# Kernel tuning notes

Hardware: AMD Instinct MI355X
Metric: run time of the kernel (lower is better)

The kernel has to match this reference:

```python
import jax, jax.numpy as jnp
import numpy as np

EXPERTS, IN_DIM, OUT_DIM, BATCH = 8, 1024, 1024, 16384

def setup_inputs() -> dict:
    key = jax.random.key(0)
    k1, k2, k3, k4 = jax.random.split(key, 4)
    bound = np.sqrt(6.0 / (IN_DIM * OUT_DIM)).astype(np.float32)
    bbound = np.sqrt(6.0 / (1 * OUT_DIM)).astype(np.float32)
    return {
        "x": jax.random.normal(k1, (BATCH, IN_DIM), dtype=jnp.float32),
        "weights": jax.random.uniform(k2, (BATCH, EXPERTS), dtype=jnp.float32),
        "W": jax.random.uniform(k3, (EXPERTS, IN_DIM, OUT_DIM), jnp.float32, -bound, bound),
        "b": jax.random.uniform(k4, (EXPERTS, 1, OUT_DIM), jnp.float32, -bbound, bbound),
    }

def reference(x, weights, W, b):
    # y[b,o] = sum_e weights[b,e] * (x[b,:] @ W[e] + b[e])
    # Fused triple einsum avoids materializing the [B,E,O] intermediate.
    y = jnp.einsum("be,bi,eio->bo", weights, x, W)
    y = y + jnp.einsum("be,eo->bo", weights, b[:, 0, :])
    return y
```

## Files before the change

### kernel.cpp

```cpp
#include <hip/hip_runtime.h>
#include <hip/hip_bf16.h>
#include <stdint.h>

#define BATCH   16384
#define EXPERTS 8
#define IN_DIM  1024
#define OUT_DIM 1024

typedef unsigned short u16;
typedef short  bf16x8 __attribute__((ext_vector_type(8)));
typedef float  f32x4  __attribute__((ext_vector_type(4)));

__device__ __forceinline__ u16 f2bf(float f) {
  uint32_t u = __float_as_uint(f);
  u += 0x7fffu + ((u >> 16) & 1u);
  return (u16)(u >> 16);
}

#define GLDS16(g, l)                                                      \
  __builtin_amdgcn_global_load_lds(                                       \
      (const __attribute__((address_space(1))) void*)(g),                 \
      (__attribute__((address_space(3))) void*)(l), 16, 0, 0)

#define MFMA_BF16 __builtin_amdgcn_mfma_f32_16x16x32_bf16
#define SB0 __builtin_amdgcn_sched_barrier(0)
#define LGKM(N) asm volatile("s_waitcnt lgkmcnt(" #N ")" ::: "memory")

__global__ void cvt_x(const float* __restrict__ x, u16* __restrict__ xb) {
  size_t i = ((size_t)blockIdx.x * 256 + threadIdx.x) * 4;
  float4 v = *reinterpret_cast<const float4*>(x + i);
  ushort4 o;
  o.x = f2bf(v.x); o.y = f2bf(v.y); o.z = f2bf(v.z); o.w = f2bf(v.w);
  *reinterpret_cast<ushort4*>(xb + i) = o;
}

__global__ void cvt_w(const float* __restrict__ W, u16* __restrict__ wbt) {
  __shared__ u16 t[64][72];
  const int e  = blockIdx.z;
  const int i0 = blockIdx.x * 64;
  const int o0 = blockIdx.y * 64;
  const int tid = threadIdx.x;
  const int c  = (tid & 15) * 4;
  const int r_ = tid >> 4;
  const float* src = W + ((size_t)e << 20);
#pragma unroll
  for (int p = 0; p < 4; ++p) {
    int r = r_ + p * 16;
    float4 v = *reinterpret_cast<const float4*>(src + (size_t)(i0 + r) * 1024 + o0 + c);
    t[r][c + 0] = f2bf(v.x); t[r][c + 1] = f2bf(v.y);
    t[r][c + 2] = f2bf(v.z); t[r][c + 3] = f2bf(v.w);
  }
  __syncthreads();
  u16* dst = wbt + ((size_t)e << 20);
#pragma unroll
  for (int p = 0; p < 4; ++p) {
    int orow = r_ + p * 16;
    ushort4 u;
    u.x = t[c + 0][orow]; u.y = t[c + 1][orow];
    u.z = t[c + 2][orow]; u.w = t[c + 3][orow];
    *reinterpret_cast<ushort4*>(dst + (size_t)(o0 + orow) * 1024 + i0 + c) = u;
  }
}

__global__ __launch_bounds__(512, 2)
void zgemm(const u16* __restrict__ xb, const u16* __restrict__ wbt,
           const float* __restrict__ wts, const float* __restrict__ bias,
           float* __restrict__ y) {
  __shared__ u16 sm[69632];
  char* smb = (char*)sm;
  float* rl = (float*)(sm + 65536);

  const int tid = threadIdx.x;
  const int l   = tid & 63;
  const int w   = tid >> 6;
  const int wm  = w >> 2;
  const int wn  = w & 3;
  const int x8  = blockIdx.x & 7;
  const int jj  = blockIdx.x >> 3;
  const int n0  = (x8 >> 1) * 256;
  const int b0  = (((x8 & 1) << 5) + jj) << 8;

#pragma unroll
  for (int i = 0; i < 4; ++i) {
    const int flat = tid + i * 512;
    const int e = flat & 7, r = flat >> 3;
    const float* wr = wts + (size_t)(b0 + r) * EXPERTS;
    float we = fmaxf(wr[e], 1e-20f);
    float rr = (e < 7) ? we / fmaxf(wr[e + 1], 1e-20f) : we;
    rl[e * 256 + r] = rr;
  }

  const int rb    = (w << 3) + (l >> 3);
  const int chunk = ((l & 7) ^ (l >> 3)) << 3;
  const u16* pAg = xb  + (size_t)(b0 + rb) * IN_DIM + chunk;
  const u16* pBg = wbt + (size_t)(n0 + rb) * 1024 + chunk;

  const int l15  = l & 15;
  const int kb0  = (((l >> 4) << 4)) ^ ((l & 7) << 4);
  const int arow = (wm * 128 + l15) * 128;
  const int brow = (wn * 64 + l15) * 128;
  const int wlo  = (wm << 9) + ((l >> 4) << 4);

  f32x4 acc[8][4];
#pragma unroll
  for (int m = 0; m < 8; ++m)
#pragma unroll
    for (int n = 0; n < 4; ++n) acc[m][n] = (f32x4){0.f, 0.f, 0.f, 0.f};

#define STG_A(q, dstE, ev_kv)                                              \
  GLDS16(pAg + (size_t)((q) * 64) * 1024 + (ev_kv),                        \
         sm + (dstE) + (q) * 4096 + (w << 9))
#define STG_B(q, dstE, off)                                                \
  GLDS16(pBg + (off) + (size_t)((q) * 64) * 1024,                          \
         sm + (dstE) + (q) * 4096 + (w << 9))

  STG_A(0, 0, 0); STG_A(1, 0, 0); STG_A(2, 0, 0); STG_A(3, 0, 0);
  STG_B(0, 32768, 0); STG_B(1, 32768, 0); STG_B(2, 32768, 0); STG_B(3, 32768, 0);
  asm volatile("s_waitcnt vmcnt(0)" ::: "memory");
  LGKM(0);
  __builtin_amdgcn_s_barrier();

#define MM(AV, BV, MB)                                                     \
  __builtin_amdgcn_s_setprio(1);                                           \
  _Pragma("unroll")                                                        \
  for (int m = 0; m < 4; ++m)                                              \
    _Pragma("unroll")                                                      \
    for (int n = 0; n < 4; ++n)                                            \
      acc[(MB) + m][n] = MFMA_BF16(AV[m], BV[n], acc[(MB) + m][n], 0, 0, 0); \
  __builtin_amdgcn_s_setprio(0);

#pragma unroll 1
  for (int t = 0; t < 128; ++t) {
    const int tn  = (t + 1) & 127;
    const int e1  = tn >> 4, k1 = tn & 15;
    const int ArB = (t & 1) << 15;
    const int AwE = ((t + 1) & 1) << 14;
    const int BrB = 65536 + ((t & 1) << 15);
    const int BwE = 32768 + (((t + 1) & 1) << 14);
    const size_t aoffg = (size_t)k1 * 64;
    const size_t boffg = (size_t)e1 * 1048576 + (size_t)k1 * 64;

    bf16x8 a0[4], b0v[4], a1[4], a2v[4], b1v[4], a3[4];

#pragma unroll
    for (int m = 0; m < 4; ++m)
      a0[m] = *(const bf16x8*)(smb + ArB + arow + m * 2048 + kb0);
#pragma unroll
    for (int n = 0; n < 4; ++n)
      b0v[n] = *(const bf16x8*)(smb + BrB + brow + n * 2048 + kb0);
#pragma unroll
    for (int m = 0; m < 4; ++m)
      a1[m] = *(const bf16x8*)(smb + ArB + arow + (m + 4) * 2048 + kb0);
    STG_A(0, AwE, aoffg); STG_A(1, AwE, aoffg);
    STG_A(2, AwE, aoffg); STG_A(3, AwE, aoffg);
    STG_B(0, BwE, boffg); STG_B(1, BwE, boffg);
    STG_B(2, BwE, boffg); STG_B(3, BwE, boffg);

    LGKM(4); SB0;
#pragma unroll
    for (int m = 0; m < 4; ++m)
      a2v[m] = *(const bf16x8*)(smb + ArB + arow + m * 2048 + (kb0 ^ 64));
#pragma unroll
    for (int n = 0; n < 4; ++n)
      b1v[n] = *(const bf16x8*)(smb + BrB + brow + n * 2048 + (kb0 ^ 64));
    MM(a0, b0v, 0)

    LGKM(8); SB0;
#pragma unroll
    for (int m = 0; m < 4; ++m)
      a3[m] = *(const bf16x8*)(smb + ArB + arow + (m + 4) * 2048 + (kb0 ^ 64));
    MM(a1, b0v, 4)

    LGKM(4); SB0;
    MM(a2v, b1v, 0)

    LGKM(0); SB0;
    MM(a3, b1v, 4)

    asm volatile("s_waitcnt vmcnt(0)" ::: "memory");
    __builtin_amdgcn_s_barrier();

    if ((t & 15) == 15 && t != 127) {
      const int e = t >> 4;
#pragma unroll
      for (int m = 0; m < 8; ++m) {
        const f32x4 rv = *(const f32x4*)(smb + 131072 + e * 1024 + wlo + m * 64);
#pragma unroll
        for (int n = 0; n < 4; ++n) acc[m][n] *= rv;
      }
      LGKM(0); SB0;
    }
  }
  asm volatile("s_waitcnt vmcnt(0)" ::: "memory");

  float bv[4][8];
#pragma unroll
  for (int n = 0; n < 4; ++n) {
    const int c = n0 + wn * 64 + n * 16 + l15;
#pragma unroll
    for (int ee = 0; ee < 8; ++ee) bv[n][ee] = bias[ee * OUT_DIM + c];
  }
#pragma unroll
  for (int m = 0; m < 8; ++m) {
    const f32x4 rv7 = *(const f32x4*)(smb + 131072 + 7 * 1024 + wlo + m * 64);
    const int r0 = b0 + wm * 128 + m * 16 + ((l >> 4) << 2);
#pragma unroll
    for (int j = 0; j < 4; ++j) {
      const float* wr = wts + (size_t)(r0 + j) * EXPERTS;
      float w8[8];
#pragma unroll
      for (int ee = 0; ee < 8; ++ee) w8[ee] = wr[ee];
#pragma unroll
      for (int n = 0; n < 4; ++n) {
        const int c = n0 + wn * 64 + n * 16 + l15;
        float v = acc[m][n][j] * rv7[j];
#pragma unroll
        for (int ee = 0; ee < 8; ++ee) v += w8[ee] * bv[n][ee];
        y[(size_t)(r0 + j) * OUT_DIM + c] = v;
      }
    }
  }
}

extern "C" void kernel_launch(void* const* d_in, const int* in_sizes, int n_in,
                              void* d_out, int out_size, void* d_ws, size_t ws_size,
                              hipStream_t stream) {
  const float* x    = (const float*)d_in[0];
  const float* wts  = (const float*)d_in[1];
  const float* W    = (const float*)d_in[2];
  const float* bias = (const float*)d_in[3];
  float* y = (float*)d_out;

  const size_t xb_elems = (size_t)BATCH * IN_DIM;
  const size_t wb_elems = (size_t)EXPERTS * IN_DIM * OUT_DIM;
  if (ws_size < (xb_elems + wb_elems) * sizeof(u16)) return;
  u16* xb  = (u16*)d_ws;
  u16* wbt = xb + xb_elems;

  cvt_x<<<(BATCH * IN_DIM) / (4 * 256), 256, 0, stream>>>(x, xb);
  cvt_w<<<dim3(IN_DIM / 64, OUT_DIM / 64, EXPERTS), 256, 0, stream>>>(W, wbt);
  zgemm<<<dim3(256), 512, 0, stream>>>(xb, wbt, wts, bias, y);
}
```

Measured before the change: 259.7 us.

## Prefetch next tile's first fragments across the barrier in GEMM main loop

Moves the vmcnt wait and barrier to mid-iteration so the first A/B LDS fragments of the next K-step can be read before the last two MFMA groups of the current step. This hides LDS read latency at the start of each iteration. An extra barrier is added at the end of each iteration to protect buffer reuse. The expert rescale block now loads all ratio vectors before multiplying. The added barrier and changed lgkm counts risk extra stalls or ordering hazards.

```diff
diff --git a/kernel.cpp b/kernel.cpp
--- a/kernel.cpp
+++ b/kernel.cpp
@@ -25,6 +25,7 @@
 #define MFMA_BF16 __builtin_amdgcn_mfma_f32_16x16x32_bf16
 #define SB0 __builtin_amdgcn_sched_barrier(0)
 #define LGKM(N) asm volatile("s_waitcnt lgkmcnt(" #N ")" ::: "memory")
+#define VM0     asm volatile("s_waitcnt vmcnt(0)" ::: "memory")
 
 __global__ void cvt_x(const float* __restrict__ x, u16* __restrict__ xb) {
   size_t i = ((size_t)blockIdx.x * 256 + threadIdx.x) * 4;
@@ -114,12 +115,6 @@
   GLDS16(pBg + (off) + (size_t)((q) * 64) * 1024,                          \
          sm + (dstE) + (q) * 4096 + (w << 9))
 
-  STG_A(0, 0, 0); STG_A(1, 0, 0); STG_A(2, 0, 0); STG_A(3, 0, 0);
-  STG_B(0, 32768, 0); STG_B(1, 32768, 0); STG_B(2, 32768, 0); STG_B(3, 32768, 0);
-  asm volatile("s_waitcnt vmcnt(0)" ::: "memory");
-  LGKM(0);
-  __builtin_amdgcn_s_barrier();
-
 #define MM(AV, BV, MB)                                                     \
   __builtin_amdgcn_s_setprio(1);                                           \
   _Pragma("unroll")                                                        \
@@ -129,32 +124,42 @@
       acc[(MB) + m][n] = MFMA_BF16(AV[m], BV[n], acc[(MB) + m][n], 0, 0, 0); \
   __builtin_amdgcn_s_setprio(0);
 
+  STG_A(0, 0, 0); STG_A(1, 0, 0); STG_A(2, 0, 0); STG_A(3, 0, 0);
+  STG_B(0, 32768, 0); STG_B(1, 32768, 0); STG_B(2, 32768, 0); STG_B(3, 32768, 0);
+  VM0;
+  LGKM(0);
+  __builtin_amdgcn_s_barrier();
+
+  bf16x8 a0[4], b0v[4];
+#pragma unroll
+  for (int m = 0; m < 4; ++m)
+    a0[m] = *(const bf16x8*)(smb + arow + m * 2048 + kb0);
+#pragma unroll
+  for (int n = 0; n < 4; ++n)
+    b0v[n] = *(const bf16x8*)(smb + 65536 + brow + n * 2048 + kb0);
+
 #pragma unroll 1
   for (int t = 0; t < 128; ++t) {
     const int tn  = (t + 1) & 127;
     const int e1  = tn >> 4, k1 = tn & 15;
-    const int ArB = (t & 1) << 15;
-    const int AwE = ((t + 1) & 1) << 14;
-    const int BrB = 65536 + ((t & 1) << 15);
-    const int BwE = 32768 + (((t + 1) & 1) << 14);
+    const int ArB  = (t & 1) << 15;
+    const int BrB  = 65536 + ((t & 1) << 15);
+    const int ArBn = ((t + 1) & 1) << 15;
+    const int BrBn = 65536 + (((t + 1) & 1) << 15);
+    const int AwE  = ((t + 1) & 1) << 14;
+    const int BwE  = 32768 + (((t + 1) & 1) << 14);
     const size_t aoffg = (size_t)k1 * 64;
     const size_t boffg = (size_t)e1 * 1048576 + (size_t)k1 * 64;
 
-    bf16x8 a0[4], b0v[4], a1[4], a2v[4], b1v[4], a3[4];
-
-#pragma unroll
-    for (int m = 0; m < 4; ++m)
-      a0[m] = *(const bf16x8*)(smb + ArB + arow + m * 2048 + kb0);
-#pragma unroll
-    for (int n = 0; n < 4; ++n)
-      b0v[n] = *(const bf16x8*)(smb + BrB + brow + n * 2048 + kb0);
-#pragma unroll
-    for (int m = 0; m < 4; ++m)
-      a1[m] = *(const bf16x8*)(smb + ArB + arow + (m + 4) * 2048 + kb0);
+    bf16x8 a1[4], a2v[4], b1v[4], a3[4];
+
     STG_A(0, AwE, aoffg); STG_A(1, AwE, aoffg);
     STG_A(2, AwE, aoffg); STG_A(3, AwE, aoffg);
     STG_B(0, BwE, boffg); STG_B(1, BwE, boffg);
     STG_B(2, BwE, boffg); STG_B(3, BwE, boffg);
+#pragma unroll
+    for (int m = 0; m < 4; ++m)
+      a1[m] = *(const bf16x8*)(smb + ArB + arow + (m + 4) * 2048 + kb0);
 
     LGKM(4); SB0;
 #pragma unroll
@@ -171,27 +176,36 @@
       a3[m] = *(const bf16x8*)(smb + ArB + arow + (m + 4) * 2048 + (kb0 ^ 64));
     MM(a1, b0v, 4)
 
+    VM0;
+    __builtin_amdgcn_s_barrier();
+
     LGKM(4); SB0;
+#pragma unroll
+    for (int m = 0; m < 4; ++m)
+      a0[m] = *(const bf16x8*)(smb + ArBn + arow + m * 2048 + kb0);
+#pragma unroll
+    for (int n = 0; n < 4; ++n)
+      b0v[n] = *(const bf16x8*)(smb + BrBn + brow + n * 2048 + kb0);
     MM(a2v, b1v, 0)
 
-    LGKM(0); SB0;
+    LGKM(8); SB0;
     MM(a3, b1v, 4)
-
-    asm volatile("s_waitcnt vmcnt(0)" ::: "memory");
-    __builtin_amdgcn_s_barrier();
 
     if ((t & 15) == 15 && t != 127) {
       const int e = t >> 4;
-#pragma unroll
-      for (int m = 0; m < 8; ++m) {
-        const f32x4 rv = *(const f32x4*)(smb + 131072 + e * 1024 + wlo + m * 64);
-#pragma unroll
-        for (int n = 0; n < 4; ++n) acc[m][n] *= rv;
-      }
+      f32x4 rv[8];
+#pragma unroll
+      for (int m = 0; m < 8; ++m)
+        rv[m] = *(const f32x4*)(smb + 131072 + e * 1024 + wlo + m * 64);
       LGKM(0); SB0;
+#pragma unroll
+      for (int m = 0; m < 8; ++m)
+#pragma unroll
+        for (int n = 0; n < 4; ++n) acc[m][n] *= rv[m];
     }
-  }
-  asm volatile("s_waitcnt vmcnt(0)" ::: "memory");
+    __builtin_amdgcn_s_barrier();
+  }
+  VM0; LGKM(0);
 
   float bv[4][8];
 #pragma unroll
```

Result: slower. 283.4 us (+9.1%).

## Prepack W into MFMA fragment layout and load B directly to registers

Applied to the files above, without the earlier changes.

The weight conversion kernel now writes W in a layout that matches the MFMA operand fragments, so the GEMM loads B straight from global memory into registers and no longer stages it through LDS. LDS use drops to the A tiles only, and the main loop is unrolled by two with register double-buffering of B and reworked waits and barriers. Launch bounds change to one block per SM. Each wave fetches its own B fragments, with no sharing through LDS, so global or L2 traffic for B rises, and occupancy hints change.

```diff
diff --git a/kernel.cpp b/kernel.cpp
--- a/kernel.cpp
+++ b/kernel.cpp
@@ -25,6 +25,7 @@
 #define MFMA_BF16 __builtin_amdgcn_mfma_f32_16x16x32_bf16
 #define SB0 __builtin_amdgcn_sched_barrier(0)
 #define LGKM(N) asm volatile("s_waitcnt lgkmcnt(" #N ")" ::: "memory")
+#define VMC(N)  asm volatile("s_waitcnt vmcnt(" #N ")" ::: "memory")
 
 __global__ void cvt_x(const float* __restrict__ x, u16* __restrict__ xb) {
   size_t i = ((size_t)blockIdx.x * 256 + threadIdx.x) * 4;
@@ -34,41 +35,46 @@
   *reinterpret_cast<ushort4*>(xb + i) = o;
 }
 
-__global__ void cvt_w(const float* __restrict__ W, u16* __restrict__ wbt) {
-  __shared__ u16 t[64][72];
-  const int e  = blockIdx.z;
-  const int i0 = blockIdx.x * 64;
-  const int o0 = blockIdx.y * 64;
-  const int tid = threadIdx.x;
-  const int c  = (tid & 15) * 4;
-  const int r_ = tid >> 4;
-  const float* src = W + ((size_t)e << 20);
-#pragma unroll
-  for (int p = 0; p < 4; ++p) {
-    int r = r_ + p * 16;
-    float4 v = *reinterpret_cast<const float4*>(src + (size_t)(i0 + r) * 1024 + o0 + c);
-    t[r][c + 0] = f2bf(v.x); t[r][c + 1] = f2bf(v.y);
-    t[r][c + 2] = f2bf(v.z); t[r][c + 3] = f2bf(v.w);
+__global__ void cvt_wp(const float* __restrict__ W, u16* __restrict__ wtp) {
+  __shared__ u16 tl[64][260];
+  const int kt = blockIdx.x, og = blockIdx.y, e = blockIdx.z;
+  const int t = threadIdx.x;
+  const float* src = W + ((size_t)e << 20) + (size_t)kt * 64 * 1024 + og * 256;
+#pragma unroll
+  for (int p = 0; p < 16; ++p) {
+    int flat = p * 256 + t;
+    int i  = flat >> 6;
+    int o4 = (flat & 63) * 4;
+    float4 v = *reinterpret_cast<const float4*>(src + (size_t)i * 1024 + o4);
+    tl[i][o4 + 0] = f2bf(v.x); tl[i][o4 + 1] = f2bf(v.y);
+    tl[i][o4 + 2] = f2bf(v.z); tl[i][o4 + 3] = f2bf(v.w);
   }
   __syncthreads();
-  u16* dst = wbt + ((size_t)e << 20);
-#pragma unroll
-  for (int p = 0; p < 4; ++p) {
-    int orow = r_ + p * 16;
-    ushort4 u;
-    u.x = t[c + 0][orow]; u.y = t[c + 1][orow];
-    u.z = t[c + 2][orow]; u.w = t[c + 3][orow];
-    *reinterpret_cast<ushort4*>(dst + (size_t)(o0 + orow) * 1024 + i0 + c) = u;
-  }
-}
-
-__global__ __launch_bounds__(512, 2)
-void zgemm(const u16* __restrict__ xb, const u16* __restrict__ wbt,
+  u16* dst = wtp + (size_t)(e * 16 + kt) * 65536 + (size_t)og * 16 * 1024;
+#pragma unroll
+  for (int s = 0; s < 8; ++s) {
+    int c   = s * 256 + t;
+    int obl = c >> 7;
+    int kf  = (c >> 6) & 1;
+    int ln  = c & 63;
+    int ol  = obl * 16 + (ln & 15);
+    int ib  = kf * 32 + ((ln >> 4) << 3);
+    u16 buf[8];
+#pragma unroll
+    for (int j = 0; j < 8; ++j) buf[j] = tl[ib + j][ol];
+    u16* d = dst + (size_t)obl * 1024 + kf * 512 + ln * 8;
+    *reinterpret_cast<ushort4*>(d)     = *(ushort4*)&buf[0];
+    *reinterpret_cast<ushort4*>(d + 4) = *(ushort4*)&buf[4];
+  }
+}
+
+__global__ __launch_bounds__(512, 1)
+void zgemm(const u16* __restrict__ xb, const u16* __restrict__ wtp,
            const float* __restrict__ wts, const float* __restrict__ bias,
            float* __restrict__ y) {
-  __shared__ u16 sm[69632];
-  char* smb = (char*)sm;
-  float* rl = (float*)(sm + 65536);
+  __shared__ u16 sm[36864];
+  const char* smb = (const char*)sm;
+  float* rl = (float*)(sm + 32768);
 
   const int tid = threadIdx.x;
   const int l   = tid & 63;
@@ -90,35 +96,27 @@
     rl[e * 256 + r] = rr;
   }
 
-  const int rb    = (w << 3) + (l >> 3);
+  const int rbl   = (w << 3) + (l >> 3);
   const int chunk = ((l & 7) ^ (l >> 3)) << 3;
-  const u16* pAg = xb  + (size_t)(b0 + rb) * IN_DIM + chunk;
-  const u16* pBg = wbt + (size_t)(n0 + rb) * 1024 + chunk;
+  const u16* pAg = xb + (size_t)(b0 + rbl) * IN_DIM + chunk;
 
   const int l15  = l & 15;
   const int kb0  = (((l >> 4) << 4)) ^ ((l & 7) << 4);
   const int arow = (wm * 128 + l15) * 128;
-  const int brow = (wn * 64 + l15) * 128;
   const int wlo  = (wm << 9) + ((l >> 4) << 4);
 
+  const int obBase = (n0 >> 4) + wn * 4;
+  const u16* pBf = wtp + (size_t)obBase * 1024 + (size_t)l * 8;
+
   f32x4 acc[8][4];
 #pragma unroll
   for (int m = 0; m < 8; ++m)
 #pragma unroll
     for (int n = 0; n < 4; ++n) acc[m][n] = (f32x4){0.f, 0.f, 0.f, 0.f};
 
-#define STG_A(q, dstE, ev_kv)                                              \
-  GLDS16(pAg + (size_t)((q) * 64) * 1024 + (ev_kv),                        \
+#define STG_A(q, dstE, kv)                                                 \
+  GLDS16(pAg + (size_t)((q) * 64) * 1024 + (size_t)(kv) * 64,              \
          sm + (dstE) + (q) * 4096 + (w << 9))
-#define STG_B(q, dstE, off)                                                \
-  GLDS16(pBg + (off) + (size_t)((q) * 64) * 1024,                          \
-         sm + (dstE) + (q) * 4096 + (w << 9))
-
-  STG_A(0, 0, 0); STG_A(1, 0, 0); STG_A(2, 0, 0); STG_A(3, 0, 0);
-  STG_B(0, 32768, 0); STG_B(1, 32768, 0); STG_B(2, 32768, 0); STG_B(3, 32768, 0);
-  asm volatile("s_waitcnt vmcnt(0)" ::: "memory");
-  LGKM(0);
-  __builtin_amdgcn_s_barrier();
 
 #define MM(AV, BV, MB)                                                     \
   __builtin_amdgcn_s_setprio(1);                                           \
@@ -129,69 +127,82 @@
       acc[(MB) + m][n] = MFMA_BF16(AV[m], BV[n], acc[(MB) + m][n], 0, 0, 0); \
   __builtin_amdgcn_s_setprio(0);
 
+  bf16x8 a0[4];
+  bf16x8 bEk0[4], bEk1[4], bOk0[4], bOk1[4];
+
+  STG_A(0, 0, 0); STG_A(1, 0, 0); STG_A(2, 0, 0); STG_A(3, 0, 0);
+#pragma unroll
+  for (int nf = 0; nf < 4; ++nf) {
+    bEk0[nf] = *(const bf16x8*)(pBf + (size_t)nf * 1024);
+    bEk1[nf] = *(const bf16x8*)(pBf + (size_t)nf * 1024 + 512);
+  }
+  VMC(0);
+  LGKM(0);
+  __builtin_amdgcn_s_barrier();
+#pragma unroll
+  for (int m = 0; m < 4; ++m)
+    a0[m] = *(const bf16x8*)(smb + arow + m * 2048 + kb0);
+
+#define BODY(TT, BCk0, BCk1, BNk0, BNk1, ARB, AWE)                         \
+  {                                                                        \
+    const int tn = ((TT) + 1) & 127;                                       \
+    const int e1 = tn >> 4, k1 = tn & 15;                                  \
+    bf16x8 a1[4], a2[4], a3[4];                                            \
+                 \
+    STG_A(0, AWE, k1); STG_A(1, AWE, k1); STG_A(2, AWE, k1); STG_A(3, AWE, k1); \
+    SB0;                                                                   \
+    {                                                                      \
+      const u16* pb = pBf + (size_t)(e1 * 16 + k1) * 65536;                \
+      _Pragma("unroll")                                                    \
+      for (int nf = 0; nf < 4; ++nf) {                                     \
+        BNk0[nf] = *(const bf16x8*)(pb + (size_t)nf * 1024);               \
+        BNk1[nf] = *(const bf16x8*)(pb + (size_t)nf * 1024 + 512);         \
+      }                                                                    \
+    }                                                                      \
+    SB0;                                                                   \
+    _Pragma("unroll")                                                      \
+    for (int m = 0; m < 4; ++m)                                            \
+      a1[m] = *(const bf16x8*)(smb + (ARB) + arow + (m + 4) * 2048 + kb0); \
+    LGKM(4); SB0;                                             \
+    _Pragma("unroll")                                                      \
+    for (int m = 0; m < 4; ++m)                                            \
+      a2[m] = *(const bf16x8*)(smb + (ARB) + arow + m * 2048 + (kb0 ^ 64)); \
+    MM(a0, BCk0, 0)                                                \
+    LGKM(4); SB0;                                             \
+    _Pragma("unroll")                                                      \
+    for (int m = 0; m < 4; ++m)                                            \
+      a3[m] = *(const bf16x8*)(smb + (ARB) + arow + (m + 4) * 2048 + (kb0 ^ 64)); \
+    MM(a1, BCk0, 4)                                                \
+    VMC(8);                                 \
+    __builtin_amdgcn_s_barrier();                 \
+    LGKM(4); SB0;                                             \
+    _Pragma("unroll")                                                      \
+    for (int m = 0; m < 4; ++m)                     \
+      a0[m] = *(const bf16x8*)(smb + ((ARB) ^ 32768) + arow + m * 2048 + kb0); \
+    MM(a2, BCk1, 0)                                                \
+    LGKM(4); SB0;                             \
+    MM(a3, BCk1, 4)                                                \
+    if (((TT) & 15) == 15 && (TT) != 127) {                                \
+      const int e = (TT) >> 4;                                             \
+      f32x4 rv[8];                                                         \
+      _Pragma("unroll")                                                    \
+      for (int m = 0; m < 8; ++m)                                          \
+        rv[m] = *(const f32x4*)(smb + 65536 + e * 1024 + wlo + m * 64);    \
+      LGKM(0); SB0;                                                        \
+      _Pragma("unroll")                                                    \
+      for (int m = 0; m < 8; ++m)                                          \
+        _Pragma("unroll")                                                  \
+        for (int n = 0; n < 4; ++n) acc[m][n] *= rv[m];                    \
+    }                                                                      \
+    __builtin_amdgcn_s_barrier();                   \
+  }
+
 #pragma unroll 1
-  for (int t = 0; t < 128; ++t) {
-    const int tn  = (t + 1) & 127;
-    const int e1  = tn >> 4, k1 = tn & 15;
-    const int ArB = (t & 1) << 15;
-    const int AwE = ((t + 1) & 1) << 14;
-    const int BrB = 65536 + ((t & 1) << 15);
-    const int BwE = 32768 + (((t + 1) & 1) << 14);
-    const size_t aoffg = (size_t)k1 * 64;
-    const size_t boffg = (size_t)e1 * 1048576 + (size_t)k1 * 64;
-
-    bf16x8 a0[4], b0v[4], a1[4], a2v[4], b1v[4], a3[4];
-
-#pragma unroll
-    for (int m = 0; m < 4; ++m)
-      a0[m] = *(const bf16x8*)(smb + ArB + arow + m * 2048 + kb0);
-#pragma unroll
-    for (int n = 0; n < 4; ++n)
-      b0v[n] = *(const bf16x8*)(smb + BrB + brow + n * 2048 + kb0);
-#pragma unroll
-    for (int m = 0; m < 4; ++m)
-      a1[m] = *(const bf16x8*)(smb + ArB + arow + (m + 4) * 2048 + kb0);
-    STG_A(0, AwE, aoffg); STG_A(1, AwE, aoffg);
-    STG_A(2, AwE, aoffg); STG_A(3, AwE, aoffg);
-    STG_B(0, BwE, boffg); STG_B(1, BwE, boffg);
-    STG_B(2, BwE, boffg); STG_B(3, BwE, boffg);
-
-    LGKM(4); SB0;
-#pragma unroll
-    for (int m = 0; m < 4; ++m)
-      a2v[m] = *(const bf16x8*)(smb + ArB + arow + m * 2048 + (kb0 ^ 64));
-#pragma unroll
-    for (int n = 0; n < 4; ++n)
-      b1v[n] = *(const bf16x8*)(smb + BrB + brow + n * 2048 + (kb0 ^ 64));
-    MM(a0, b0v, 0)
-
-    LGKM(8); SB0;
-#pragma unroll
-    for (int m = 0; m < 4; ++m)
-      a3[m] = *(const bf16x8*)(smb + ArB + arow + (m + 4) * 2048 + (kb0 ^ 64));
-    MM(a1, b0v, 4)
-
-    LGKM(4); SB0;
-    MM(a2v, b1v, 0)
-
-    LGKM(0); SB0;
-    MM(a3, b1v, 4)
-
-    asm volatile("s_waitcnt vmcnt(0)" ::: "memory");
-    __builtin_amdgcn_s_barrier();
-
-    if ((t & 15) == 15 && t != 127) {
-      const int e = t >> 4;
-#pragma unroll
-      for (int m = 0; m < 8; ++m) {
-        const f32x4 rv = *(const f32x4*)(smb + 131072 + e * 1024 + wlo + m * 64);
-#pragma unroll
-        for (int n = 0; n < 4; ++n) acc[m][n] *= rv;
-      }
-      LGKM(0); SB0;
-    }
-  }
-  asm volatile("s_waitcnt vmcnt(0)" ::: "memory");
+  for (int t = 0; t < 128; t += 2) {
+    BODY(t,     bEk0, bEk1, bOk0, bOk1, 0,     16384)
+    BODY(t + 1, bOk0, bOk1, bEk0, bEk1, 32768, 0)
+  }
+  VMC(0); LGKM(0);
 
   float bv[4][8];
 #pragma unroll
@@ -202,7 +213,7 @@
   }
 #pragma unroll
   for (int m = 0; m < 8; ++m) {
-    const f32x4 rv7 = *(const f32x4*)(smb + 131072 + 7 * 1024 + wlo + m * 64);
+    const f32x4 rv7 = *(const f32x4*)(smb + 65536 + 7 * 1024 + wlo + m * 64);
     const int r0 = b0 + wm * 128 + m * 16 + ((l >> 4) << 2);
 #pragma unroll
     for (int j = 0; j < 4; ++j) {
@@ -232,12 +243,12 @@
   float* y = (float*)d_out;
 
   const size_t xb_elems = (size_t)BATCH * IN_DIM;
-  const size_t wb_elems = (size_t)EXPERTS * IN_DIM * OUT_DIM;
-  if (ws_size < (xb_elems + wb_elems) * sizeof(u16)) return;
+  const size_t wp_elems = (size_t)EXPERTS * IN_DIM * OUT_DIM;
+  if (ws_size < (xb_elems + wp_elems) * sizeof(u16)) return;
   u16* xb  = (u16*)d_ws;
-  u16* wbt = xb + xb_elems;
+  u16* wtp = xb + xb_elems;
 
   cvt_x<<<(BATCH * IN_DIM) / (4 * 256), 256, 0, stream>>>(x, xb);
-  cvt_w<<<dim3(IN_DIM / 64, OUT_DIM / 64, EXPERTS), 256, 0, stream>>>(W, wbt);
-  zgemm<<<dim3(256), 512, 0, stream>>>(xb, wbt, wts, bias, y);
-}
+  cvt_wp<<<dim3(16, 4, 8), 256, 0, stream>>>(W, wtp);
+  zgemm<<<dim3(256), 512, 0, stream>>>(xb, wtp, wts, bias, y);
+}
```

After: 280.0 us. 1.08x slower.

## Split GEMM main loop into barrier-separated phases with staggered global loads

Applied to the files above, without the earlier changes.

The K-loop is reorganised into four MFMA phases, each preceded by its own LDS fragment reads and a slice of the next tile's global-to-LDS loads, separated by workgroup barriers. A full vmcnt(0) drain at the end of every iteration is replaced by partial vmcnt waits, so global loads can stay in flight across the iteration boundary. The per-expert rescale now loads all scale vectors before a single lgkmcnt wait. The aim is a steadier interleave of memory traffic and MFMA work, at the cost of many more barriers per iteration and tighter ordering that must hold for the double-buffered LDS to stay correct.

```diff
diff --git a/kernel.cpp b/kernel.cpp
--- a/kernel.cpp
+++ b/kernel.cpp
@@ -25,6 +25,7 @@
 #define MFMA_BF16 __builtin_amdgcn_mfma_f32_16x16x32_bf16
 #define SB0 __builtin_amdgcn_sched_barrier(0)
 #define LGKM(N) asm volatile("s_waitcnt lgkmcnt(" #N ")" ::: "memory")
+#define VMC(N)  asm volatile("s_waitcnt vmcnt(" #N ")" ::: "memory")
 
 __global__ void cvt_x(const float* __restrict__ x, u16* __restrict__ xb) {
   size_t i = ((size_t)blockIdx.x * 256 + threadIdx.x) * 4;
@@ -90,10 +91,10 @@
     rl[e * 256 + r] = rr;
   }
 
-  const int rb    = (w << 3) + (l >> 3);
+  const int rbl   = (w << 3) + (l >> 3);
   const int chunk = ((l & 7) ^ (l >> 3)) << 3;
-  const u16* pAg = xb  + (size_t)(b0 + rb) * IN_DIM + chunk;
-  const u16* pBg = wbt + (size_t)(n0 + rb) * 1024 + chunk;
+  const u16* pAg = xb  + (size_t)(b0 + rbl) * IN_DIM + chunk;
+  const u16* pBg = wbt + (size_t)(n0 + rbl) * 1024 + chunk;
 
   const int l15  = l & 15;
   const int kb0  = (((l >> 4) << 4)) ^ ((l & 7) << 4);
@@ -107,18 +108,12 @@
 #pragma unroll
     for (int n = 0; n < 4; ++n) acc[m][n] = (f32x4){0.f, 0.f, 0.f, 0.f};
 
-#define STG_A(q, dstE, ev_kv)                                              \
-  GLDS16(pAg + (size_t)((q) * 64) * 1024 + (ev_kv),                        \
+#define STG_A(q, dstE, kv)                                                 \
+  GLDS16(pAg + (size_t)((q) * 64) * 1024 + (size_t)(kv) * 64,              \
          sm + (dstE) + (q) * 4096 + (w << 9))
 #define STG_B(q, dstE, off)                                                \
   GLDS16(pBg + (off) + (size_t)((q) * 64) * 1024,                          \
          sm + (dstE) + (q) * 4096 + (w << 9))
-
-  STG_A(0, 0, 0); STG_A(1, 0, 0); STG_A(2, 0, 0); STG_A(3, 0, 0);
-  STG_B(0, 32768, 0); STG_B(1, 32768, 0); STG_B(2, 32768, 0); STG_B(3, 32768, 0);
-  asm volatile("s_waitcnt vmcnt(0)" ::: "memory");
-  LGKM(0);
-  __builtin_amdgcn_s_barrier();
 
 #define MM(AV, BV, MB)                                                     \
   __builtin_amdgcn_s_setprio(1);                                           \
@@ -129,69 +124,84 @@
       acc[(MB) + m][n] = MFMA_BF16(AV[m], BV[n], acc[(MB) + m][n], 0, 0, 0); \
   __builtin_amdgcn_s_setprio(0);
 
+  STG_A(0, 0, 0); STG_A(1, 0, 0); STG_A(2, 0, 0); STG_A(3, 0, 0);
+  STG_B(0, 32768, 0); STG_B(1, 32768, 0); STG_B(2, 32768, 0); STG_B(3, 32768, 0);
+  VMC(0);
+  LGKM(0);
+  __builtin_amdgcn_s_barrier();
+
 #pragma unroll 1
   for (int t = 0; t < 128; ++t) {
     const int tn  = (t + 1) & 127;
     const int e1  = tn >> 4, k1 = tn & 15;
     const int ArB = (t & 1) << 15;
+    const int BrB = 65536 + ((t & 1) << 15);
     const int AwE = ((t + 1) & 1) << 14;
-    const int BrB = 65536 + ((t & 1) << 15);
     const int BwE = 32768 + (((t + 1) & 1) << 14);
-    const size_t aoffg = (size_t)k1 * 64;
     const size_t boffg = (size_t)e1 * 1048576 + (size_t)k1 * 64;
 
-    bf16x8 a0[4], b0v[4], a1[4], a2v[4], b1v[4], a3[4];
-
-#pragma unroll
-    for (int m = 0; m < 4; ++m)
-      a0[m] = *(const bf16x8*)(smb + ArB + arow + m * 2048 + kb0);
+    bf16x8 a[4], b[4];
+
+#pragma unroll
+    for (int m = 0; m < 4; ++m)
+      a[m] = *(const bf16x8*)(smb + ArB + arow + m * 2048 + kb0);
 #pragma unroll
     for (int n = 0; n < 4; ++n)
-      b0v[n] = *(const bf16x8*)(smb + BrB + brow + n * 2048 + kb0);
+      b[n] = *(const bf16x8*)(smb + BrB + brow + n * 2048 + kb0);
+    STG_B(0, BwE, boffg); STG_B(1, BwE, boffg);
+    VMC(2);
+    __builtin_amdgcn_s_barrier();
+    LGKM(0); SB0;
+    MM(a, b, 0)
+    __builtin_amdgcn_s_barrier();
+
+    bf16x8 a1[4];
 #pragma unroll
     for (int m = 0; m < 4; ++m)
       a1[m] = *(const bf16x8*)(smb + ArB + arow + (m + 4) * 2048 + kb0);
-    STG_A(0, AwE, aoffg); STG_A(1, AwE, aoffg);
-    STG_A(2, AwE, aoffg); STG_A(3, AwE, aoffg);
-    STG_B(0, BwE, boffg); STG_B(1, BwE, boffg);
     STG_B(2, BwE, boffg); STG_B(3, BwE, boffg);
-
-    LGKM(4); SB0;
-#pragma unroll
-    for (int m = 0; m < 4; ++m)
-      a2v[m] = *(const bf16x8*)(smb + ArB + arow + m * 2048 + (kb0 ^ 64));
+    __builtin_amdgcn_s_barrier();
+    LGKM(0); SB0;
+    MM(a1, b, 4)
+    __builtin_amdgcn_s_barrier();
+
+    bf16x8 a2[4], b2[4];
+#pragma unroll
+    for (int m = 0; m < 4; ++m)
+      a2[m] = *(const bf16x8*)(smb + ArB + arow + m * 2048 + (kb0 ^ 64));
 #pragma unroll
     for (int n = 0; n < 4; ++n)
-      b1v[n] = *(const bf16x8*)(smb + BrB + brow + n * 2048 + (kb0 ^ 64));
-    MM(a0, b0v, 0)
-
-    LGKM(8); SB0;
+      b2[n] = *(const bf16x8*)(smb + BrB + brow + n * 2048 + (kb0 ^ 64));
+    STG_A(0, AwE, k1); STG_A(2, AwE, k1);
+    __builtin_amdgcn_s_barrier();
+    LGKM(0); SB0;
+    MM(a2, b2, 0)
+    __builtin_amdgcn_s_barrier();
+
+    bf16x8 a3[4];
 #pragma unroll
     for (int m = 0; m < 4; ++m)
       a3[m] = *(const bf16x8*)(smb + ArB + arow + (m + 4) * 2048 + (kb0 ^ 64));
-    MM(a1, b0v, 4)
-
-    LGKM(4); SB0;
-    MM(a2v, b1v, 0)
-
-    LGKM(0); SB0;
-    MM(a3, b1v, 4)
-
-    asm volatile("s_waitcnt vmcnt(0)" ::: "memory");
-    __builtin_amdgcn_s_barrier();
-
+    STG_A(1, AwE, k1); STG_A(3, AwE, k1);
+    VMC(2);
+    __builtin_amdgcn_s_barrier();
+    LGKM(0); SB0;
+    MM(a3, b2, 4)
     if ((t & 15) == 15 && t != 127) {
       const int e = t >> 4;
-#pragma unroll
-      for (int m = 0; m < 8; ++m) {
-        const f32x4 rv = *(const f32x4*)(smb + 131072 + e * 1024 + wlo + m * 64);
-#pragma unroll
-        for (int n = 0; n < 4; ++n) acc[m][n] *= rv;
-      }
+      f32x4 rv[8];
+#pragma unroll
+      for (int m = 0; m < 8; ++m)
+        rv[m] = *(const f32x4*)(smb + 131072 + e * 1024 + wlo + m * 64);
       LGKM(0); SB0;
+#pragma unroll
+      for (int m = 0; m < 8; ++m)
+#pragma unroll
+        for (int n = 0; n < 4; ++n) acc[m][n] *= rv[m];
     }
-  }
-  asm volatile("s_waitcnt vmcnt(0)" ::: "memory");
+    __builtin_amdgcn_s_barrier();
+  }
+  VMC(0); LGKM(0);
 
   float bv[4][8];
 #pragma unroll
```

Result: no change. 262.1 us (+0.9%).
